# Kernel optimization log

Measured on AMD Instinct MI355X. Metric: run time of the kernel, lower is better.

## Reference

```python
import jax, jax.numpy as jnp
import numpy as np

M_CENTER = 3.0  # diagonal value of the 'centers' matrix
OUT_HW = (513, 513)  # original input spatial size (input_shape in torch forward)


def _conv(x, w, dilation=1, padding=0):
    return jax.lax.conv_general_dilated(
        x, w, window_strides=(1, 1),
        padding=[(padding, padding), (padding, padding)],
        rhs_dilation=(dilation, dilation),
        dimension_numbers=("NCHW", "OIHW", "NCHW"))


def _resize(x, hw):
    return jax.image.resize(x, (x.shape[0], x.shape[1], hw[0], hw[1]), method="bilinear")


def _head(low_level, out, pw, w0, w1, w2, w3, pool_w, aproj_w, cw1, cw2, cb2):
    # DeepLabHeadV3Plus (BN folded to identity at inference: gamma=1, beta=0, mean=0, var=1)
    ll = jax.nn.relu(_conv(low_level, pw))                      # [N,48,129,129]
    branches = [jax.nn.relu(_conv(out, w0))]                    # 1x1 branch
    for w, d in zip((w1, w2, w3), (6, 12, 18)):
        branches.append(jax.nn.relu(_conv(out, w, dilation=d, padding=d)))
    gp = jnp.mean(out, axis=(2, 3), keepdims=True)              # AdaptiveAvgPool2d(1)
    gp = jax.nn.relu(_conv(gp, pool_w))
    gp = jnp.broadcast_to(gp, branches[0].shape)                # bilinear upsample of 1x1 == broadcast
    branches.append(gp)
    y = jax.nn.relu(_conv(jnp.concatenate(branches, axis=1), aproj_w))  # [N,256,33,33]
    y = _resize(y, (ll.shape[2], ll.shape[3]))                  # -> 129x129
    y = jnp.concatenate([ll, y], axis=1)                        # [N,304,129,129]
    y = jax.nn.relu(_conv(y, cw1, padding=1))
    y = _conv(y, cw2) + cb2[None, :, None, None]                # [N,C,129,129]
    return y


def _forward_single(x):
    # x: [N,C,129,129] head logits. Upsample, then squared-distance to diagonal centers (m*I).
    x = _resize(x, OUT_HW)                                      # [N,C,513,513]
    C = x.shape[1]
    features_out = jnp.transpose(x, (0, 2, 3, 1))               # NHWC, as in torch
    # dist2mean[...,c] = -sum_j (f_j - m*1[j==c])^2 = -(|f|^2 - 2*m*f_c + m^2)
    sumsq = jnp.sum(x * x, axis=1, keepdims=True)
    logits = 2.0 * M_CENTER * x - sumsq - M_CENTER * M_CENTER   # [N,C,513,513]
    centers = M_CENTER * jnp.eye(C, dtype=x.dtype)
    return logits, centers, features_out


def _kaiming(key, shape):
    fan_in = shape[1] * shape[2] * shape[3]
    return jax.random.normal(key, shape, jnp.float32) * np.sqrt(2.0 / fan_in)


def _head_params(key, num_classes):
    ks = jax.random.split(key, 10)
    return dict(
        pw=_kaiming(ks[0], (48, 256, 1, 1)),
        w0=_kaiming(ks[1], (256, 2048, 1, 1)),
        w1=_kaiming(ks[2], (256, 2048, 3, 3)),
        w2=_kaiming(ks[3], (256, 2048, 3, 3)),
        w3=_kaiming(ks[4], (256, 2048, 3, 3)),
        pool_w=_kaiming(ks[5], (256, 2048, 1, 1)),
        aproj_w=_kaiming(ks[6], (256, 1280, 1, 1)),
        cw1=_kaiming(ks[7], (256, 304, 3, 3)),
        cw2=_kaiming(ks[8], (num_classes, 256, 1, 1)),
        cb2=jnp.zeros((num_classes,), jnp.float32),
    )


def setup_inputs() -> dict:
    key = jax.random.key(0)
    k_ll, k_out, k_h0, k_h1 = jax.random.split(key, 4)
    inp = {
        "low_level": jax.random.normal(k_ll, (2, 256, 129, 129), jnp.float32),
        "out": jax.random.normal(k_out, (2, 2048, 33, 33), jnp.float32),
    }
    for pref, k, nc in (("h0_", k_h0, 16), ("h1_", k_h1, 17)):
        for name, v in _head_params(k, nc).items():
            inp[pref + name] = v
    return inp


def reference(low_level, out,
              h0_pw, h0_w0, h0_w1, h0_w2, h0_w3, h0_pool_w, h0_aproj_w, h0_cw1, h0_cw2, h0_cb2,
              h1_pw, h1_w0, h1_w1, h1_w2, h1_w3, h1_pool_w, h1_aproj_w, h1_cw1, h1_cw2, h1_cb2):
    x0 = _head(low_level, out, h0_pw, h0_w0, h0_w1, h0_w2, h0_w3, h0_pool_w, h0_aproj_w, h0_cw1, h0_cw2, h0_cb2)
    x1 = _head(low_level, out, h1_pw, h1_w0, h1_w1, h1_w2, h1_w3, h1_pool_w, h1_aproj_w, h1_cw1, h1_cw2, h1_cb2)
    l0, c0, f0 = _forward_single(x0)
    l1, c1, f1 = _forward_single(x1)
    return (l0, l1, c0, c1, f0, f1)
```

## Files before the change

### kernel.cpp

```cpp
#include <hip/hip_runtime.h>

#define TPB 256

typedef _Float16 f16;
typedef __attribute__((ext_vector_type(8))) _Float16 f16x8;
typedef __attribute__((ext_vector_type(16))) float f32x16;

#define GLD_LDS(g, l) __builtin_amdgcn_global_load_lds( \
    (const __attribute__((address_space(1))) void*)(g), \
    (__attribute__((address_space(3))) void*)(l), 16, 0, 0)

__global__ __launch_bounds__(TPB)
void tcz_k(const float* __restrict__ aspp, const float* __restrict__ ll,
           f16* __restrict__ Xa, f16* __restrict__ Xll, float* __restrict__ brz)
{
    const int bid = blockIdx.x;
    const int tid = threadIdx.x;
    if (bid >= 12816) {
        const int z = bid - 12816;
        float4 zv = {0.f, 0.f, 0.f, 0.f};
        float4* p = (float4*)(brz + (long)z * 4096 + tid * 16);
        p[0] = zv; p[1] = zv; p[2] = zv; p[3] = zv;
        return;
    }
    const float* src; f16* dst; int C, HW, ldk, pT, cT, bb;
    if (bid < 4480) {
        src = aspp; dst = Xa; C = 2048; HW = 1089; ldk = 2048;
        pT = bid % 35; cT = (bid / 35) % 64; bb = bid / 2240;
    } else {
        const int b2 = bid - 4480;
        src = ll; dst = Xll; C = 256; HW = 16641; ldk = 256;
        pT = b2 % 521; cT = (b2 / 521) % 8; bb = b2 / 4168;
    }
    __shared__ float t32[32 * 33];
#pragma unroll
    for (int pass = 0; pass < 4; ++pass) {
        const int ch = tid / 32 + pass * 8;
        const int px = tid % 32;
        const int c = cT * 32 + ch, p = pT * 32 + px;
        float v = 0.f;
        if (c < C && p < HW) v = src[((long)bb * C + c) * HW + p];
        t32[ch * 33 + px] = v;
    }
    __syncthreads();
#pragma unroll
    for (int pass = 0; pass < 4; ++pass) {
        const int px = tid / 32 + pass * 8;
        const int ch = tid % 32;
        const int p = pT * 32 + px, c = cT * 32 + ch;
        if (p < HW && c < C)
            dst[((long)bb * HW + p) * ldk + c] = (f16)t32[ch * 33 + px];
    }
}

__global__ __launch_bounds__(TPB)
void tcr_k(const float* __restrict__ src, f16* __restrict__ dst, int C, int HW, int ldk)
{
    __shared__ float t32[32 * 33];
    const int pT = blockIdx.x, cT = blockIdx.y, bb = blockIdx.z;
    const int tid = threadIdx.x;
#pragma unroll
    for (int pass = 0; pass < 4; ++pass) {
        const int ch = tid / 32 + pass * 8;
        const int px = tid % 32;
        const int c = cT * 32 + ch, p = pT * 32 + px;
        float v = 0.f;
        if (c < C && p < HW) v = fmaxf(src[((long)bb * C + c) * HW + p], 0.f);
        t32[ch * 33 + px] = v;
    }
    __syncthreads();
#pragma unroll
    for (int pass = 0; pass < 4; ++pass) {
        const int px = tid / 32 + pass * 8;
        const int ch = tid % 32;
        const int p = pT * 32 + px, c = cT * 32 + ch;
        if (p < HW && c < C)
            dst[((long)bb * HW + p) * ldk + c] = (f16)t32[ch * 33 + px];
    }
}

__global__ __launch_bounds__(TPB)
void gpool_k(const float* __restrict__ in, float* __restrict__ gp, int HW, float inv)
{
    const int bc = blockIdx.x;
    const float* p = in + (size_t)bc * HW;
    float s = 0.f;
    for (int i = threadIdx.x; i < HW; i += TPB) s += p[i];
#pragma unroll
    for (int off = 32; off > 0; off >>= 1) s += __shfl_down(s, off, 64);
    __shared__ float red[4];
    if ((threadIdx.x & 63) == 0) red[threadIdx.x >> 6] = s;
    __syncthreads();
    if (threadIdx.x == 0) gp[bc] = (red[0] + red[1] + red[2] + red[3]) * inv;
}

__global__ __launch_bounds__(TPB)
void gemv1_k(const float* __restrict__ pw0, const float* __restrict__ pw1,
             const float* __restrict__ gp, float* __restrict__ gpr2)
{
    const int bh = blockIdx.x & 3;
    const int cgrp = blockIdx.x >> 2;
    const int b = bh & 1;
    const float* w = (bh >> 1) ? pw1 : pw0;
    const int c = cgrp * 16 + (threadIdx.x >> 4);
    const int kl = threadIdx.x & 15;
    const float* g = gp + (size_t)b * 2048;
    float4 acc = {0.f, 0.f, 0.f, 0.f};
    for (int k = kl * 4; k < 2048; k += 64) {
        const float4 wv = *(const float4*)&w[(size_t)c * 2048 + k];
        const float4 gv = *(const float4*)&g[k];
        acc.x = fmaf(wv.x, gv.x, acc.x);
        acc.y = fmaf(wv.y, gv.y, acc.y);
        acc.z = fmaf(wv.z, gv.z, acc.z);
        acc.w = fmaf(wv.w, gv.w, acc.w);
    }
    float s = (acc.x + acc.y) + (acc.z + acc.w);
#pragma unroll
    for (int o = 8; o; o >>= 1) s += __shfl_xor(s, o, 16);
    if (kl == 0) gpr2[bh * 256 + c] = fmaxf(s, 0.f);
}

__global__ __launch_bounds__(TPB)
void gemv2_k(const float* __restrict__ ap0, const float* __restrict__ ap1,
             const float* __restrict__ gpr2, float* __restrict__ gpc2)
{
    const int bh = blockIdx.x & 3;
    const int cgrp = blockIdx.x >> 2;
    const float* w = (bh >> 1) ? ap1 : ap0;
    const int c = cgrp * 16 + (threadIdx.x >> 4);
    const int kl = threadIdx.x & 15;
    const float* g = gpr2 + bh * 256;
    float4 acc = {0.f, 0.f, 0.f, 0.f};
    for (int k = kl * 4; k < 256; k += 64) {
        const float4 wv = *(const float4*)&w[(size_t)c * 1280 + 1024 + k];
        const float4 gv = *(const float4*)&g[k];
        acc.x = fmaf(wv.x, gv.x, acc.x);
        acc.y = fmaf(wv.y, gv.y, acc.y);
        acc.z = fmaf(wv.z, gv.z, acc.z);
        acc.w = fmaf(wv.w, gv.w, acc.w);
    }
    float s = (acc.x + acc.y) + (acc.z + acc.w);
#pragma unroll
    for (int o = 8; o; o >>= 1) s += __shfl_xor(s, o, 16);
    if (kl == 0) gpc2[bh * 256 + c] = s;
}

struct PackJob { const float* w; f16* dst; int Cout, CinUse, CinSrc, T, coP, KB, start; };
struct PackParams { PackJob j[14]; };

__global__ __launch_bounds__(TPB)
void packw_mega(PackParams P, float* __restrict__ guard)
{
    const int bid = blockIdx.x;
    const int tid = threadIdx.x;
    if (bid >= 4832) {
        float4 zv = {0.f, 0.f, 0.f, 0.f};
        float4* p = (float4*)(guard + tid * 16);
        p[0] = zv; p[1] = zv; p[2] = zv; p[3] = zv;
        return;
    }
    int ji = 0;
#pragma unroll
    for (int t = 1; t < 14; ++t) if (bid >= P.j[t].start) ji = t;
    PackJob J;
    switch (ji) {
        case 0:  J = P.j[0];  break;
        case 1:  J = P.j[1];  break;
        case 2:  J = P.j[2];  break;
        case 3:  J = P.j[3];  break;
        case 4:  J = P.j[4];  break;
        case 5:  J = P.j[5];  break;
        case 6:  J = P.j[6];  break;
        case 7:  J = P.j[7];  break;
        case 8:  J = P.j[8];  break;
        case 9:  J = P.j[9];  break;
        case 10: J = P.j[10]; break;
        case 11: J = P.j[11]; break;
        case 12: J = P.j[12]; break;
        default: J = P.j[13]; break;
    }
    const int local = bid - J.start;
    const int kb = local % J.KB;
    const int coT = local / J.KB;
    const int T = J.T;
    __shared__ float tile[16 * 577];
    const int RL = 64 * T;
    const int n = 16 * RL;
    for (int idx = tid; idx < n; idx += TPB) {
        const int row = idx / RL;
        const int jj = idx - row * RL;
        const int co = coT * 16 + row;
        const int k = kb * 64 + jj / T;
        float v = 0.f;
        if (co < J.Cout && k < J.CinUse)
            v = J.w[((long)co * J.CinSrc + kb * 64) * T + jj];
        tile[row * 577 + jj] = v;
    }
    __syncthreads();
    const int nst = 128 * T;
    for (int idx = tid; idx < nst; idx += TPB) {
        const int g = idx & 7;
        const int t = (idx >> 3) % T;
        const int co = idx / (8 * T);
        f16x8 hv;
#pragma unroll
        for (int e = 0; e < 8; ++e)
            hv[e] = (f16)tile[co * 577 + (g * 8 + e) * T + t];
        *(f16x8*)&J.dst[(((long)t * J.KB + kb) * J.coP + coT * 16 + co) * 64 + g * 8] = hv;
    }
}

template <int OUTMODE, int ZMAP, int RELUOUT, int BIAS>
__global__ __launch_bounds__(TPB, 4)
void mconv(const f16* __restrict__ X, const f16* __restrict__ Wp,
           const f16* __restrict__ guard, void* __restrict__ out_,
           const float* __restrict__ gpc,
           int Cinp, int Cout, int H, int W, int kss_, int dl_,
           int kbPerTap, int tapCnt_,
           long xHstr, long wHstr, long oHstr, long outBStride,
           int coP, int ldOut, int NM, int NBH, int NZ)
{
    __shared__ char SH[32768];
    const int tid = threadIdx.x;

    int wg;
    {
        const int orig = blockIdx.x, nwg = gridDim.x;
        const int q = nwg >> 3, r = nwg & 7;
        const int xcd = orig & 7, off = orig >> 3;
        wg = (xcd < r ? xcd * (q + 1) : r * (q + 1) + (xcd - r) * q) + off;
    }
    const int mt = wg % NM; wg /= NM;
    const int bh = wg % NBH; wg /= NBH;
    const int z  = wg % NZ;
    const int nt = wg / NZ;
    const int b = bh & 1, hd = bh >> 1;
    const int co0 = mt * 128;
    const int NP = H * W;
    const long xBstr = (long)NP * Cinp;

    int kss = kss_, dl = dl_, tapStart = 0, tapCnt = tapCnt_;
    long woff = (long)hd * wHstr, ooff = (long)hd * oHstr;
    int p0 = nt * 128, pMax = NP;
    if (ZMAP == 1) {
        int br, grp;
        if (z == 0) { br = 0; grp = 1; kss = 1; dl = 1; tapStart = 0; tapCnt = 1; }
        else { br = 1 + (z - 1) / 3; grp = (z - 1) % 3;
               kss = 3; dl = (br == 1) ? 6 : (br == 2 ? 12 : 18);
               tapStart = grp * 3; tapCnt = 3; }
        woff += (br == 0) ? 0L : (br == 1 ? 524288L : (br == 2 ? 5242880L : 9961472L));
        ooff += (long)br * 278784L;
        const int dy0 = (kss == 1) ? 0 : (grp - 1) * dl;
        const int yLo = max(0, -dy0), yHi = min(H, H - dy0);
        p0 = yLo * W + nt * 128;
        pMax = yHi * W;
        if (p0 >= pMax) return;
    }
    const int half = kss >> 1;
    const int y0t = p0 / W, y1t = min(p0 + 127, pMax - 1) / W;

    int taps[9]; int nval = 0;
    for (int t = 0; t < tapCnt; ++t) {
        const int tp = tapStart + t;
        const int ky = tp / kss;
        const int dy = (ky - half) * dl;
        if (ZMAP == 1 || (y1t + dy >= 0 && y0t + dy < H)) taps[nval++] = tp;
    }
    if (nval == 0) return;

    const int srow = tid >> 3;
    const int sslot = tid & 7;
    int aofs[4];
#pragma unroll
    for (int q = 0; q < 4; ++q) {
        const int row = q * 32 + srow;
        aofs[q] = row * 64 + ((sslot ^ (row & 7)) << 3);
    }
    const long coStr = (long)coP * 64;

    const int lane = tid & 63, wid = tid >> 6;
    const int wm = wid >> 1, wn = wid & 1;
    const int r32 = lane & 31, hh = lane >> 5;
    const int arow0 = wm * 64 + r32, arow1 = arow0 + 32;
    const int brow0 = wn * 64 + r32, brow1 = brow0 + 32;
    const int abase0 = arow0 * 128, abase1 = arow1 * 128;
    const int bbase0 = 16384 + brow0 * 128, bbase1 = 16384 + brow1 * 128;
    const int ax0 = (arow0 & 7), ax1 = (arow1 & 7);
    const int bx0 = (brow0 & 7), bx1 = (brow1 & 7);

    f32x16 acc[2][2];
#pragma unroll
    for (int i = 0; i < 2; ++i)
#pragma unroll
        for (int j = 0; j < 2; ++j) acc[i][j] = (f32x16)(0.f);

    const f16* Pr[4];
    for (int ti = 0; ti < nval; ++ti) {
        const int tp = taps[ti];
        const int ky = tp / kss, kx = tp - ky * kss;
        const int dy = (ky - half) * dl, dx = (kx - half) * dl;
#pragma unroll
        for (int q = 0; q < 4; ++q) {
            const int row = q * 32 + srow;
            const int p = p0 + row;
            bool v = p < pMax;
            const int py = v ? p / W : 0;
            const int px = v ? p - py * W : 0;
            const int sy = py + dy, sx = px + dx;
            v = v && ((unsigned)sy < (unsigned)H) && ((unsigned)sx < (unsigned)W);
            const int swz = (sslot ^ (row & 7)) << 3;
            Pr[q] = v ? (X + (long)b * xBstr + (long)hd * xHstr
                           + ((long)sy * W + sx) * (long)Cinp + swz)
                      : (guard + swz);
        }
        const f16* Wt = Wp + woff + ((long)tp * kbPerTap * coP + (long)co0) * 64;
        for (int kb = 0; kb < kbPerTap; ++kb) {
            __syncthreads();
            const f16* wsrc = Wt + (long)kb * coStr;
            const long kcol = (long)kb << 6;
            GLD_LDS(wsrc + aofs[0], SH + (tid << 4));
            GLD_LDS(wsrc + aofs[1], SH + 4096 + (tid << 4));
            GLD_LDS(wsrc + aofs[2], SH + 8192 + (tid << 4));
            GLD_LDS(wsrc + aofs[3], SH + 12288 + (tid << 4));
            GLD_LDS(Pr[0] + kcol, SH + 16384 + (tid << 4));
            GLD_LDS(Pr[1] + kcol, SH + 20480 + (tid << 4));
            GLD_LDS(Pr[2] + kcol, SH + 24576 + (tid << 4));
            GLD_LDS(Pr[3] + kcol, SH + 28672 + (tid << 4));
            __syncthreads();
            __builtin_amdgcn_s_setprio(1);
#pragma unroll
            for (int kh = 0; kh < 4; ++kh) {
                const int g = kh * 2 + hh;
                const f16x8 a0 = *(const f16x8*)(SH + abase0 + ((g ^ ax0) << 4));
                const f16x8 a1 = *(const f16x8*)(SH + abase1 + ((g ^ ax1) << 4));
                const f16x8 b0 = *(const f16x8*)(SH + bbase0 + ((g ^ bx0) << 4));
                const f16x8 b1 = *(const f16x8*)(SH + bbase1 + ((g ^ bx1) << 4));
                acc[0][0] = __builtin_amdgcn_mfma_f32_32x32x16_f16(a0, b0, acc[0][0], 0, 0, 0);
                acc[0][1] = __builtin_amdgcn_mfma_f32_32x32x16_f16(a0, b1, acc[0][1], 0, 0, 0);
                acc[1][0] = __builtin_amdgcn_mfma_f32_32x32x16_f16(a1, b0, acc[1][0], 0, 0, 0);
                acc[1][1] = __builtin_amdgcn_mfma_f32_32x32x16_f16(a1, b1, acc[1][1], 0, 0, 0);
            }
            __builtin_amdgcn_s_setprio(0);
        }
    }

    const long outB = (long)b * outBStride + ooff;
    const float* gpcp = BIAS ? (gpc + (long)(b + 2 * hd) * 256) : nullptr;
#pragma unroll
    for (int mi = 0; mi < 2; ++mi)
#pragma unroll
    for (int ni = 0; ni < 2; ++ni)
#pragma unroll
    for (int j = 0; j < 16; ++j) {
        const int m = wm * 64 + mi * 32 + 4 * hh + (j & 3) + 8 * (j >> 2);
        const int n = wn * 64 + ni * 32 + r32;
        const int co = co0 + m;
        const int p = p0 + n;
        if (co < Cout && p < pMax) {
            float v = acc[mi][ni][j];
            if (BIAS) v += gpcp[co];
            if (RELUOUT) v = fmaxf(v, 0.f);
            if (OUTMODE == 0)      ((float*)out_)[outB + (long)co * NP + p] = v;
            else if (OUTMODE == 1) ((f16*)out_)[outB + (long)co * NP + p] = (f16)v;
            else if (OUTMODE == 3) ((f16*)out_)[outB + (long)p * ldOut + co] = (f16)v;
            else atomicAdd(&((float*)out_)[outB + (long)co * NP + p], v);
        }
    }
}

__global__ __launch_bounds__(TPB)
void ups2pad_k(const f16* __restrict__ ybx, f16* __restrict__ ccx)
{
    const int idx = blockIdx.x * TPB + threadIdx.x;
    if (idx >= 4 * 16641 * 34) return;
    const int s = idx / (16641 * 34);
    const int rem = idx - s * (16641 * 34);
    const int p = rem / 34;
    const int cg = rem - p * 34;
    if (cg >= 32) {
        f16x8 zv = (f16x8)(f16)0.f;
        *(f16x8*)(ccx + ((long)s * 16641 + p) * 320 + 304 + (cg - 32) * 8) = zv;
        return;
    }
    const int oy = p / 129, ox = p % 129;
    const float sc = 33.0f / 129.0f;
    const float sx = (ox + 0.5f) * sc - 0.5f;
    const float sy = (oy + 0.5f) * sc - 0.5f;
    int ix0 = (int)floorf(sx), iy0 = (int)floorf(sy);
    const float fx = sx - ix0, fy = sy - iy0;
    int ix1 = min(32, max(0, ix0 + 1)); ix0 = min(32, max(0, ix0));
    int iy1 = min(32, max(0, iy0 + 1)); iy0 = min(32, max(0, iy0));
    const f16* base = ybx + (long)s * 1089 * 256 + cg * 8;
    const f16x8 v00 = *(const f16x8*)(base + ((long)iy0 * 33 + ix0) * 256);
    const f16x8 v01 = *(const f16x8*)(base + ((long)iy0 * 33 + ix1) * 256);
    const f16x8 v10 = *(const f16x8*)(base + ((long)iy1 * 33 + ix0) * 256);
    const f16x8 v11 = *(const f16x8*)(base + ((long)iy1 * 33 + ix1) * 256);
    f16x8 r;
#pragma unroll
    for (int e = 0; e < 8; ++e) {
        const float a0 = (float)v00[e] + ((float)v01[e] - (float)v00[e]) * fx;
        const float a1 = (float)v10[e] + ((float)v11[e] - (float)v10[e]) * fx;
        r[e] = (f16)(a0 + (a1 - a0) * fy);
    }
    *(f16x8*)(ccx + ((long)s * 16641 + p) * 320 + 48 + cg * 8) = r;
}

__global__ __launch_bounds__(TPB)
void conv1x1_m(const f16* __restrict__ c1o2,
               const float* __restrict__ w0, const float* __restrict__ w1,
               const float* __restrict__ b0, const float* __restrict__ b1,
               float* __restrict__ xb2)
{
    const int h = blockIdx.z;
    const int nc = h ? 17 : 16;
    const float* w = h ? w1 : w0;
    const float* bias = h ? b1 : b0;
    __shared__ float wsm[256 * 17];
    __shared__ float bsm[17];
    const int tid = threadIdx.x;
    for (int l = tid; l < 256 * 17; l += TPB) {
        const int k = l / 17, c = l - k * 17;
        wsm[l] = (c < nc) ? w[(size_t)c * 256 + k] : 0.f;
    }
    if (tid < nc) bsm[tid] = bias[tid];
    __syncthreads();
    const int b = blockIdx.y;
    const int p = blockIdx.x * TPB + tid;
    if (p >= 16641) return;
    const f16* inB = c1o2 + (long)h * 8520192 + (long)b * 4260096 + p;
    float acc[17];
#pragma unroll
    for (int c = 0; c < 17; ++c) acc[c] = 0.f;
    for (int k = 0; k < 256; ++k) {
        const float x = (float)inB[(size_t)k * 16641];
#pragma unroll
        for (int c = 0; c < 17; ++c) acc[c] = fmaf(wsm[k * 17 + c], x, acc[c]);
    }
    float* oB = xb2 + (h ? 532512L : 0L) + ((long)b * nc) * 16641 + p;
#pragma unroll
    for (int c = 0; c < 17; ++c)
        if (c < nc) oB[(size_t)c * 16641] = acc[c] + bsm[c];
}

__global__ __launch_bounds__(TPB)
void final_m(const float* __restrict__ xb2, float* __restrict__ o)
{
    const int idx = blockIdx.x * TPB + threadIdx.x;
    if (idx >= 2 * 526338) return;
    const int hd = idx / 526338;
    int r = idx - hd * 526338;
    const int ox = r % 513; r /= 513;
    const int oy = r % 513;
    const int b = r / 513;
    const int nc = hd ? 17 : 16;
    const long HW = 513L * 513L;
    const float sc = 129.0f / 513.0f;
    const float sx = (ox + 0.5f) * sc - 0.5f;
    const float sy = (oy + 0.5f) * sc - 0.5f;
    int ix0 = (int)floorf(sx), iy0 = (int)floorf(sy);
    const float fx = sx - ix0, fy = sy - iy0;
    int ix1 = min(128, max(0, ix0 + 1)); ix0 = min(128, max(0, ix0));
    int iy1 = min(128, max(0, iy0 + 1)); iy0 = min(128, max(0, iy0));
    const float* xb = xb2 + (hd ? 532512L : 0L) + (size_t)b * nc * 16641;
    const int i00 = iy0 * 129 + ix0, i01 = iy0 * 129 + ix1;
    const int i10 = iy1 * 129 + ix0, i11 = iy1 * 129 + ix1;
    float* logits = o + (hd ? 8421408L : 0L);
    float* feats  = o + (hd ? 25791107L : 17369699L);
    float v[17];
    float ss = 0.f;
#pragma unroll
    for (int c = 0; c < 17; ++c) {
        if (c < nc) {
            const float* s = xb + (size_t)c * 16641;
            const float a0 = s[i00] + (s[i01] - s[i00]) * fx;
            const float a1 = s[i10] + (s[i11] - s[i10]) * fx;
            const float vv = a0 + (a1 - a0) * fy;
            v[c] = vv;
            ss = fmaf(vv, vv, ss);
        }
    }
    const long pix = (long)oy * 513 + ox;
#pragma unroll
    for (int c = 0; c < 17; ++c)
        if (c < nc)
            logits[((size_t)b * nc + c) * HW + pix] = fmaf(6.f, v[c], -ss - 9.f);
    float* f = feats + ((size_t)b * HW + pix) * nc;
#pragma unroll
    for (int c = 0; c < 17; ++c)
        if (c < nc) f[c] = v[c];
}

__global__ void centers_k(float* __restrict__ c0, float* __restrict__ c1)
{
    const int t = blockIdx.x * 64 + threadIdx.x;
    if (t < 256) c0[t] = (t / 16 == t % 16) ? 3.f : 0.f;
    const int u = t - 256;
    if (u >= 0 && u < 289) c1[u] = (u / 17 == u % 17) ? 3.f : 0.f;
}

extern "C" void kernel_launch(void* const* d_in, const int* in_sizes, int n_in,
                              void* d_out, int out_size, void* d_ws, size_t ws_size,
                              hipStream_t stream)
{
    const float* low_level = (const float*)d_in[0];
    const float* aspp_in   = (const float*)d_in[1];
    float* ws = (float*)d_ws;
    float* o  = (float*)d_out;

    float* GUARDF  = ws + 0;
    f16*   GUARD   = (f16*)GUARDF;
    f16*   Apack2  = (f16*)(ws + 4096);
    f16*   C1O2    = (f16*)(ws + 4096);
    f16*   AprojP2 = (f16*)(ws + 14684160);
    f16*   Cw1P2   = (f16*)(ws + 14946304);
    f16*   LlP2    = (f16*)(ws + 15683584);
    f16*   Xa      = (f16*)(ws + 15716352);
    float* BRacc2  = ws + 17946624;
    f16*   BRX2    = (f16*)(ws + 22407168);
    f16*   YBX2    = (f16*)(ws + 24637440);
    float* XB2     = ws + 25195008;
    float* GP      = ws + 26293314;
    float* GPC2    = ws + 26297410;
    float* GPR2    = ws + 26298434;

    f16*   CCX2    = (f16*)(o + 0);
    f16*   Xll     = (f16*)(o + 10650240);

    const long C0o = 17369154, C1oo = 17369410;

    tcz_k<<<13905, TPB, 0, stream>>>(aspp_in, low_level, Xa, Xll, BRacc2);
    gpool_k<<<4096, TPB, 0, stream>>>(aspp_in, GP, 1089, 1.0f / 1089.0f);
    gemv1_k<<<64, TPB, 0, stream>>>(
        (const float*)d_in[2 + 5], (const float*)d_in[2 + 10 + 5], GP, GPR2);
    gemv2_k<<<64, TPB, 0, stream>>>(
        (const float*)d_in[2 + 6], (const float*)d_in[2 + 10 + 6], GPR2, GPC2);

    PackParams P;
    int start = 0;
    for (int h = 0; h < 2; ++h) {
        const float* pw    = (const float*)d_in[2 + h * 10 + 0];
        const float* w0    = (const float*)d_in[2 + h * 10 + 1];
        const float* w1    = (const float*)d_in[2 + h * 10 + 2];
        const float* w2    = (const float*)d_in[2 + h * 10 + 3];
        const float* w3    = (const float*)d_in[2 + h * 10 + 4];
        const float* aproj = (const float*)d_in[2 + h * 10 + 6];
        const float* cw1   = (const float*)d_in[2 + h * 10 + 7];
        f16* Ap = Apack2 + (long)h * 14680064;
        const PackJob jobs[7] = {
            { w0,    Ap,                          256, 2048, 2048, 1, 256, 32, 0 },
            { w1,    Ap + 524288,                 256, 2048, 2048, 9, 256, 32, 0 },
            { w2,    Ap + 5242880,                256, 2048, 2048, 9, 256, 32, 0 },
            { w3,    Ap + 9961472,                256, 2048, 2048, 9, 256, 32, 0 },
            { aproj, AprojP2 + (long)h * 262144,  256, 1024, 1280, 1, 256, 16, 0 },
            { cw1,   Cw1P2 + (long)h * 737280,    256,  304,  304, 9, 256,  5, 0 },
            { pw,    LlP2 + (long)h * 32768,       48,  256,  256, 1, 128,  4, 0 },
        };
        for (int t = 0; t < 7; ++t) {
            P.j[h * 7 + t] = jobs[t];
            P.j[h * 7 + t].start = start;
            start += jobs[t].KB * (jobs[t].coP / 16);
        }
    }
    packw_mega<<<4833, TPB, 0, stream>>>(P, GUARDF);

    mconv<2, 1, 0, 0><<<720, TPB, 0, stream>>>(
        Xa, Apack2, GUARD, BRacc2, nullptr, 2048, 256, 33, 33, 3, 1,
        32, 0, 0L, 14680064L, 2230272L, 1115136L, 256, 0, 2, 4, 10);
    tcr_k<<<dim3(35, 32, 4), TPB, 0, stream>>>(BRacc2, BRX2, 1024, 1089, 1024);
    mconv<3, 0, 1, 1><<<72, TPB, 0, stream>>>(
        BRX2, AprojP2, GUARD, YBX2, GPC2, 1024, 256, 33, 33, 1, 1,
        16, 1, 2230272L, 262144L, 557568L, 278784L, 256, 256, 2, 4, 1);
    mconv<3, 0, 1, 0><<<524, TPB, 0, stream>>>(
        Xll, LlP2, GUARD, CCX2, nullptr, 256, 48, 129, 129, 1, 1,
        4, 1, 0L, 32768L, 10650240L, 5325120L, 128, 320, 1, 4, 1);
    ups2pad_k<<<8841, TPB, 0, stream>>>(YBX2, CCX2);
    mconv<1, 0, 1, 0><<<1048, TPB, 0, stream>>>(
        CCX2, Cw1P2, GUARD, C1O2, nullptr, 320, 256, 129, 129, 3, 1,
        5, 9, 10650240L, 737280L, 8520192L, 4260096L, 256, 0, 2, 4, 1);
    conv1x1_m<<<dim3(66, 2, 2), TPB, 0, stream>>>(C1O2,
        (const float*)d_in[2 + 8], (const float*)d_in[2 + 10 + 8],
        (const float*)d_in[2 + 9], (const float*)d_in[2 + 10 + 9], XB2);
    final_m<<<4113, TPB, 0, stream>>>(XB2, o);
    centers_k<<<9, 64, 0, stream>>>(o + C0o, o + C1oo);
}
```

Baseline: 640.1 us.

## Replace atomic branch accumulation with per-group fp16 partials reduced in transpose

The dilated ASPP conv previously accumulated its three tap-group contributions per branch into a zeroed fp32 buffer (output mode 2, likely atomics), which needed a zeroing pass inside tcz_k. Each tap group now writes its own fp16 partial slice, and the transpose/ReLU kernel sums the valid groups per row before converting. This removes the zero-fill blocks and the atomic contention. In exchange the workspace grows, the transpose kernel reads up to three partials, and partial sums are rounded to fp16 before being added.

```diff
diff --git a/kernel.cpp b/kernel.cpp
--- a/kernel.cpp
+++ b/kernel.cpp
@@ -12,17 +12,10 @@
 
 __global__ __launch_bounds__(TPB)
 void tcz_k(const float* __restrict__ aspp, const float* __restrict__ ll,
-           f16* __restrict__ Xa, f16* __restrict__ Xll, float* __restrict__ brz)
+           f16* __restrict__ Xa, f16* __restrict__ Xll)
 {
     const int bid = blockIdx.x;
     const int tid = threadIdx.x;
-    if (bid >= 12816) {
-        const int z = bid - 12816;
-        float4 zv = {0.f, 0.f, 0.f, 0.f};
-        float4* p = (float4*)(brz + (long)z * 4096 + tid * 16);
-        p[0] = zv; p[1] = zv; p[2] = zv; p[3] = zv;
-        return;
-    }
     const float* src; f16* dst; int C, HW, ldk, pT, cT, bb;
     if (bid < 4480) {
         src = aspp; dst = Xa; C = 2048; HW = 1089; ldk = 2048;
@@ -54,18 +47,38 @@
 }
 
 __global__ __launch_bounds__(TPB)
-void tcr_k(const float* __restrict__ src, f16* __restrict__ dst, int C, int HW, int ldk)
+void tcr_k(const f16* __restrict__ part, f16* __restrict__ dst)
 {
     __shared__ float t32[32 * 33];
     const int pT = blockIdx.x, cT = blockIdx.y, bb = blockIdx.z;
     const int tid = threadIdx.x;
+    const int br = cT >> 3;
+    const f16* pb = part + (long)bb * 2787840;
 #pragma unroll
     for (int pass = 0; pass < 4; ++pass) {
         const int ch = tid / 32 + pass * 8;
         const int px = tid % 32;
-        const int c = cT * 32 + ch, p = pT * 32 + px;
+        const int c = cT * 32 + ch;
+        const int cl = c & 255;
+        const int p = pT * 32 + px;
         float v = 0.f;
-        if (c < C && p < HW) v = fmaxf(src[((long)bb * C + c) * HW + p], 0.f);
+        if (p < 1089) {
+            if (br == 0) {
+                v = (float)pb[(long)cl * 1089 + p];
+            } else {
+                const int dl = 6 * br;
+                const int y = p / 33;
+                const int s0 = 1 + 3 * (br - 1);
+#pragma unroll
+                for (int g = 0; g < 3; ++g) {
+                    const int dy0 = (g - 1) * dl;
+                    const int yLo = max(0, -dy0), yHi = min(33, 33 - dy0);
+                    if (y >= yLo && y < yHi)
+                        v += (float)pb[((long)(s0 + g) * 256 + cl) * 1089 + p];
+                }
+            }
+            v = fmaxf(v, 0.f);
+        }
         t32[ch * 33 + px] = v;
     }
     __syncthreads();
@@ -74,8 +87,8 @@
         const int px = tid / 32 + pass * 8;
         const int ch = tid % 32;
         const int p = pT * 32 + px, c = cT * 32 + ch;
-        if (p < HW && c < C)
-            dst[((long)bb * HW + p) * ldk + c] = (f16)t32[ch * 33 + px];
+        if (p < 1089)
+            dst[((long)bb * 1089 + p) * 1024 + c] = (f16)t32[ch * 33 + px];
     }
 }
 
@@ -249,7 +262,7 @@
                kss = 3; dl = (br == 1) ? 6 : (br == 2 ? 12 : 18);
                tapStart = grp * 3; tapCnt = 3; }
         woff += (br == 0) ? 0L : (br == 1 ? 524288L : (br == 2 ? 5242880L : 9961472L));
-        ooff += (long)br * 278784L;
+        ooff += (long)z * 278784L;
         const int dy0 = (kss == 1) ? 0 : (grp - 1) * dl;
         const int yLo = max(0, -dy0), yHi = min(H, H - dy0);
         p0 = yLo * W + nt * 128;
@@ -515,20 +528,20 @@
     f16*   Cw1P2   = (f16*)(ws + 14946304);
     f16*   LlP2    = (f16*)(ws + 15683584);
     f16*   Xa      = (f16*)(ws + 15716352);
-    float* BRacc2  = ws + 17946624;
-    f16*   BRX2    = (f16*)(ws + 22407168);
-    f16*   YBX2    = (f16*)(ws + 24637440);
-    float* XB2     = ws + 25195008;
-    float* GP      = ws + 26293314;
-    float* GPC2    = ws + 26297410;
-    float* GPR2    = ws + 26298434;
+    f16*   BRpart  = (f16*)(ws + 17946624);
+    f16*   BRX2    = (f16*)(ws + 23522304);
+    f16*   YBX2    = (f16*)(ws + 25752576);
+    float* XB2     = ws + 26310144;
+    float* GP      = ws + 27408450;
+    float* GPC2    = ws + 27412546;
+    float* GPR2    = ws + 27413570;
 
     f16*   CCX2    = (f16*)(o + 0);
     f16*   Xll     = (f16*)(o + 10650240);
 
     const long C0o = 17369154, C1oo = 17369410;
 
-    tcz_k<<<13905, TPB, 0, stream>>>(aspp_in, low_level, Xa, Xll, BRacc2);
+    tcz_k<<<12816, TPB, 0, stream>>>(aspp_in, low_level, Xa, Xll);
     gpool_k<<<4096, TPB, 0, stream>>>(aspp_in, GP, 1089, 1.0f / 1089.0f);
     gemv1_k<<<64, TPB, 0, stream>>>(
         (const float*)d_in[2 + 5], (const float*)d_in[2 + 10 + 5], GP, GPR2);
@@ -563,10 +576,10 @@
     }
     packw_mega<<<4833, TPB, 0, stream>>>(P, GUARDF);
 
-    mconv<2, 1, 0, 0><<<720, TPB, 0, stream>>>(
-        Xa, Apack2, GUARD, BRacc2, nullptr, 2048, 256, 33, 33, 3, 1,
-        32, 0, 0L, 14680064L, 2230272L, 1115136L, 256, 0, 2, 4, 10);
-    tcr_k<<<dim3(35, 32, 4), TPB, 0, stream>>>(BRacc2, BRX2, 1024, 1089, 1024);
+    mconv<1, 1, 0, 0><<<720, TPB, 0, stream>>>(
+        Xa, Apack2, GUARD, BRpart, nullptr, 2048, 256, 33, 33, 3, 1,
+        32, 0, 0L, 14680064L, 5575680L, 2787840L, 256, 0, 2, 4, 10);
+    tcr_k<<<dim3(35, 32, 4), TPB, 0, stream>>>(BRpart, BRX2);
     mconv<3, 0, 1, 1><<<72, TPB, 0, stream>>>(
         BRX2, AprojP2, GUARD, YBX2, GPC2, 1024, 256, 33, 33, 1, 1,
         16, 1, 2230272L, 262144L, 557568L, 278784L, 256, 256, 2, 4, 1);
```

New measurement: 637.6 us. No clear change (-0.4%).
